# Kernel optimization log

Hardware: AMD Instinct MI355X
Metric: run time of the kernel (lower is better)

The kernel has to match this reference:

```python
import jax, jax.numpy as jnp
import numpy as np

D = 256      # d_model
NH = 8       # heads
HD = D // NH # head dim = 32
NL = 4       # feature levels
NP = 4       # sampling points per head per level
DFF = 1024   # ffn hidden
LAYERS = 6
SHAPES = [(48, 48), (24, 24), (12, 12), (6, 6)]


def setup_inputs() -> dict:
    key = jax.random.key(0)
    ks = jax.random.split(key, 20)
    bs = 2
    inp = {}
    for i, (h, w) in enumerate(SHAPES):
        inp[f"src{i}"] = jax.random.normal(ks[i], (bs, D, h, w), jnp.float32)
        inp[f"pos{i}"] = jax.random.normal(ks[4 + i], (bs, D, h, w), jnp.float32)

    def p(k, shape, s=0.02):
        return jax.random.normal(k, shape, jnp.float32) * s

    inp["level_embed"] = p(ks[8], (NL, D), 1.0)
    inp["Wv"] = p(ks[9], (LAYERS, D, D))
    inp["bv"] = jnp.zeros((LAYERS, D))
    inp["Woff"] = p(ks[10], (LAYERS, D, NH * NL * NP * 2), 0.001)
    inp["boff"] = p(ks[11], (LAYERS, NH * NL * NP * 2), 0.5)
    inp["Wa"] = p(ks[12], (LAYERS, D, NH * NL * NP))
    inp["ba"] = jnp.zeros((LAYERS, NH * NL * NP))
    inp["Wo"] = p(ks[13], (LAYERS, D, D))
    inp["bo"] = jnp.zeros((LAYERS, D))
    inp["g1"] = jnp.ones((LAYERS, D))
    inp["beta1"] = jnp.zeros((LAYERS, D))
    inp["W1"] = p(ks[14], (LAYERS, D, DFF))
    inp["bf1"] = jnp.zeros((LAYERS, DFF))
    inp["W2"] = p(ks[15], (LAYERS, DFF, D))
    inp["bf2"] = jnp.zeros((LAYERS, D))
    inp["g2"] = jnp.ones((LAYERS, D))
    inp["beta2"] = jnp.zeros((LAYERS, D))
    return inp


def _ln(x, g, b):
    m = x.mean(-1, keepdims=True)
    v = ((x - m) ** 2).mean(-1, keepdims=True)
    return (x - m) / jnp.sqrt(v + 1e-5) * g + b


def _bilinear(value, loc, H, W):
    # value: (bs, NH, H*W, HD); loc: (bs, Len, NH, NP, 2) in [0,1]
    # grid_sample, align_corners=False, zero padding
    bs, Len, nh, P, _ = loc.shape
    x = loc[..., 0] * W - 0.5
    y = loc[..., 1] * H - 0.5
    x0 = jnp.floor(x)
    y0 = jnp.floor(y)
    lx = x - x0
    ly = y - y0
    x0i = x0.astype(jnp.int32)
    y0i = y0.astype(jnp.int32)
    out = jnp.zeros((bs, nh, Len, P, value.shape[-1]), value.dtype)
    for dy, dx, w in ((0, 0, (1 - lx) * (1 - ly)), (0, 1, lx * (1 - ly)),
                      (1, 0, (1 - lx) * ly), (1, 1, lx * ly)):
        xi = x0i + dx
        yi = y0i + dy
        valid = (xi >= 0) & (xi < W) & (yi >= 0) & (yi < H)
        idx = jnp.clip(yi, 0, H - 1) * W + jnp.clip(xi, 0, W - 1)  # (bs,Len,NH,P)
        idx_t = idx.transpose(0, 2, 1, 3).reshape(bs, nh, Len * P)
        v = jnp.take_along_axis(value, idx_t[..., None], axis=2)
        v = v.reshape(bs, nh, Len, P, -1)
        wm = (w * valid).transpose(0, 2, 1, 3)  # (bs,NH,Len,P)
        out = out + v * wm[..., None]
    return out


def _msda(q, src, ref, shapes, starts, Wv, bv, Woff, boff, Wa, ba, Wo, bo):
    bs, Len, _ = q.shape
    value = (src @ Wv + bv).reshape(bs, Len, NH, HD)
    off = (q @ Woff + boff).reshape(bs, Len, NH, NL, NP, 2)
    attn = jax.nn.softmax((q @ Wa + ba).reshape(bs, Len, NH, NL * NP), -1)
    attn = attn.reshape(bs, Len, NH, NL, NP)
    acc = jnp.zeros((bs, NH, Len, HD), q.dtype)
    for lv, (H, W) in enumerate(shapes):
        norm = jnp.array([W, H], q.dtype)
        loc = ref[None, :, None, None, :] + off[:, :, :, lv] / norm  # (bs,Len,NH,NP,2)
        v = value[:, starts[lv]:starts[lv] + H * W].transpose(0, 2, 1, 3)
        samp = _bilinear(v, loc, H, W)  # (bs,NH,Len,NP,HD)
        acc = acc + (samp * attn[:, :, :, lv].transpose(0, 2, 1, 3)[..., None]).sum(3)
    return acc.transpose(0, 2, 1, 3).reshape(bs, Len, D) @ Wo + bo


def _encode(srcs, poss, level_embed, Wv, bv, Woff, boff, Wa, ba, Wo, bo,
            g1, beta1, W1, bf1, W2, bf2, g2, beta2):
    shapes = [(s.shape[2], s.shape[3]) for s in srcs]
    bs = srcs[0].shape[0]
    src_flat = jnp.concatenate(
        [s.reshape(bs, D, -1).transpose(0, 2, 1) for s in srcs], 1)
    pos_flat = jnp.concatenate(
        [p.reshape(bs, D, -1).transpose(0, 2, 1) + level_embed[i][None, None]
         for i, p in enumerate(poss)], 1)
    starts = np.cumsum([0] + [h * w for h, w in shapes])[:-1]
    # reference points (masks are all-zero so valid_ratios == 1)
    refs = []
    for (H, W) in shapes:
        ry, rx = jnp.meshgrid(jnp.linspace(0.5, H - 0.5, H) / H,
                              jnp.linspace(0.5, W - 0.5, W) / W, indexing='ij')
        refs.append(jnp.stack([rx.reshape(-1), ry.reshape(-1)], -1))
    ref = jnp.concatenate(refs, 0)  # (Len, 2)

    out = src_flat
    for l in range(LAYERS):
        q = out + pos_flat
        out2 = _msda(q, out, ref, shapes, starts, Wv[l], bv[l], Woff[l],
                     boff[l], Wa[l], ba[l], Wo[l], bo[l])
        out = _ln(out + out2, g1[l], beta1[l])
        h = jax.nn.relu(out @ W1[l] + bf1[l])
        out = _ln(out + h @ W2[l] + bf2[l], g2[l], beta2[l])
    return out, shapes, starts


def reference(src0, src1, src2, src3, pos0, pos1, pos2, pos3, level_embed,
              Wv, bv, Woff, boff, Wa, ba, Wo, bo,
              g1, beta1, W1, bf1, W2, bf2, g2, beta2):
    memory, shapes, starts = _encode(
        [src0, src1, src2, src3], [pos0, pos1, pos2, pos3], level_embed,
        Wv, bv, Woff, boff, Wa, ba, Wo, bo,
        g1, beta1, W1, bf1, W2, bf2, g2, beta2)
    spatial_shapes = jnp.array(shapes, jnp.int32)
    level_start_index = jnp.array(np.asarray(starts), jnp.int32)
    return memory, spatial_shapes, level_start_index
```

## Files before the change

### kernel.cpp

```cpp
#include <hip/hip_runtime.h>
#include <math.h>

#define D_MODEL 256
#define NHEAD 8
#define HDIM 32
#define NLVL 4
#define NPTS 4
#define DFF 1024
#define NLAYERS 6
#define LEN 3060
#define BS 2
#define MROWS (BS * LEN)
#define MPAD 6144

typedef __attribute__((ext_vector_type(8))) short bf16x8;
typedef __attribute__((ext_vector_type(4))) float f32x4;

__device__ __forceinline__ unsigned short f2bf(float f) {
    union { float f; unsigned u; } v; v.f = f;
    unsigned r = v.u + 0x7FFF + ((v.u >> 16) & 1);
    return (unsigned short)(r >> 16);
}
__device__ __forceinline__ float bf2f(unsigned short s) {
    union { unsigned u; float f; } v; v.u = ((unsigned)s) << 16;
    return v.f;
}

#define GLDS(gp, lp) __builtin_amdgcn_global_load_lds(                        \
    (const __attribute__((address_space(1))) void*)(gp),                      \
    (__attribute__((address_space(3))) void*)(lp), 16, 0, 0)

__global__ __launch_bounds__(256) void flatten_kernel(
    const float* __restrict__ s0, const float* __restrict__ s1,
    const float* __restrict__ s2, const float* __restrict__ s3,
    const float* __restrict__ p0, const float* __restrict__ p1,
    const float* __restrict__ p2, const float* __restrict__ p3,
    const float* __restrict__ lemb,
    float* __restrict__ out, unsigned short* __restrict__ outbf,
    unsigned short* __restrict__ qbf, float* __restrict__ pos)
{
    int gid = blockIdx.x * 256 + threadIdx.x;
    if (gid >= MROWS * D_MODEL) return;
    int d  = gid & (D_MODEL - 1);
    int bt = gid >> 8;
    int b  = (bt >= LEN) ? 1 : 0;
    int t  = bt - b * LEN;

    int lv, li, hw;
    const float* sp; const float* pp;
    if (t < 2304)      { lv = 0; li = t;        hw = 2304; sp = s0; pp = p0; }
    else if (t < 2880) { lv = 1; li = t - 2304; hw = 576;  sp = s1; pp = p1; }
    else if (t < 3024) { lv = 2; li = t - 2880; hw = 144;  sp = s2; pp = p2; }
    else               { lv = 3; li = t - 3024; hw = 36;   sp = s3; pp = p3; }

    size_t si = (size_t)(b * D_MODEL + d) * hw + li;
    float v = sp[si];
    float pv = pp[si] + lemb[lv * D_MODEL + d];
    out[gid]   = v;
    outbf[gid] = f2bf(v);
    qbf[gid]   = f2bf(v + pv);
    pos[gid]   = pv;
}

__global__ __launch_bounds__(256) void wconv_kernel(
    const float* __restrict__ Wv, const float* __restrict__ Woff,
    const float* __restrict__ Wa, const float* __restrict__ Wo,
    const float* __restrict__ W1, const float* __restrict__ W2,
    unsigned short* __restrict__ Wv_t, unsigned short* __restrict__ Woffa_t,
    unsigned short* __restrict__ Wo_t, unsigned short* __restrict__ W1_t,
    unsigned short* __restrict__ W2_t)
{
    __shared__ float tile[32][33];
    int bid = blockIdx.x;
    int layer = bid / 736, r = bid % 736;
    const float* src; unsigned short* dst;
    int N, tk, tn, dstRowOff = 0, dstLd;
    if (r < 64)       { src = Wv  + layer*65536;  dst = Wv_t   + layer*65536;  N = 256;  int t2 = r;       tk = t2 >> 3; tn = t2 & 7;  dstLd = 256;  }
    else if (r < 128) { src = Woff+ layer*65536;  dst = Woffa_t+ layer*98304;  N = 256;  int t2 = r - 64;  tk = t2 >> 3; tn = t2 & 7;  dstLd = 256;  }
    else if (r < 160) { src = Wa  + layer*32768;  dst = Woffa_t+ layer*98304;  N = 128;  int t2 = r - 128; tk = t2 >> 2; tn = t2 & 3;  dstLd = 256;  dstRowOff = 256; }
    else if (r < 224) { src = Wo  + layer*65536;  dst = Wo_t   + layer*65536;  N = 256;  int t2 = r - 160; tk = t2 >> 3; tn = t2 & 7;  dstLd = 256;  }
    else if (r < 480) { src = W1  + layer*262144; dst = W1_t   + layer*262144; N = 1024; int t2 = r - 224; tk = t2 >> 5; tn = t2 & 31; dstLd = 256;  }
    else              { src = W2  + layer*262144; dst = W2_t   + layer*262144; N = 256;  int t2 = r - 480; tk = t2 >> 3; tn = t2 & 7;  dstLd = 1024; }
    int k0 = tk * 32, n0 = tn * 32;
    int tx = threadIdx.x & 31, ty = threadIdx.x >> 5;
    #pragma unroll
    for (int i = 0; i < 4; ++i)
        tile[ty + i*8][tx] = src[(size_t)(k0 + ty + i*8) * N + n0 + tx];
    __syncthreads();
    #pragma unroll
    for (int i = 0; i < 4; ++i)
        dst[(size_t)(dstRowOff + n0 + ty + i*8) * dstLd + k0 + tx] =
            f2bf(tile[tx][ty + i*8]);
}

__device__ __forceinline__ void gemm_core(
    const unsigned short* __restrict__ A, const unsigned short* __restrict__ Bt,
    int row0, int col0, int K, char* smem, f32x4 (&acc)[4][2])
{
    const int tid  = threadIdx.x;
    const int lane = tid & 63, wave = tid >> 6;
    const int wm = wave >> 1, wn = wave & 1;
    const int l15 = lane & 15, l4 = lane >> 4;

    const unsigned short* aS[4]; const unsigned short* bS[2];
    int aD[4], bD[2];
    #pragma unroll
    for (int i = 0; i < 4; ++i) {
        int c = i*256 + tid, q = c >> 7, r = c & 127;
        aS[i] = A + (size_t)(row0 + r) * K + q*8;
        aD[i] = c * 16;
    }
    #pragma unroll
    for (int i = 0; i < 2; ++i) {
        int c = i*256 + tid, q = c >> 6, n = c & 63;
        bS[i] = Bt + (size_t)(col0 + n) * K + q*8;
        bD[i] = 16384 + c * 16;
    }

    int aOff[4][2], bOff[2][2];
    #pragma unroll
    for (int mf = 0; mf < 4; ++mf)
        #pragma unroll
        for (int s = 0; s < 2; ++s)
            aOff[mf][s] = ((s*4 + l4)*128 + wm*64 + mf*16 + l15) * 16;
    #pragma unroll
    for (int nf = 0; nf < 2; ++nf)
        #pragma unroll
        for (int s = 0; s < 2; ++s)
            bOff[nf][s] = 16384 + ((s*4 + l4)*64 + wn*32 + nf*16 + l15) * 16;

    #pragma unroll
    for (int i = 0; i < 4; ++i) GLDS(aS[i], smem + aD[i]);
    #pragma unroll
    for (int i = 0; i < 2; ++i) GLDS(bS[i], smem + bD[i]);
    __syncthreads();

    const int nt = K >> 6;
    for (int t = 0; t < nt; ++t) {
        const int bo = (t & 1) * 24576;
        if (t + 1 < nt) {
            const int nbo = ((t + 1) & 1) * 24576;
            const int k0 = (t + 1) << 6;
            #pragma unroll
            for (int i = 0; i < 4; ++i) GLDS(aS[i] + k0, smem + nbo + aD[i]);
            #pragma unroll
            for (int i = 0; i < 2; ++i) GLDS(bS[i] + k0, smem + nbo + bD[i]);
        }
        #pragma unroll
        for (int s = 0; s < 2; ++s) {
            bf16x8 bfr[2];
            #pragma unroll
            for (int nf = 0; nf < 2; ++nf)
                bfr[nf] = *(const bf16x8*)(smem + bo + bOff[nf][s]);
            #pragma unroll
            for (int mf = 0; mf < 4; ++mf) {
                bf16x8 afr = *(const bf16x8*)(smem + bo + aOff[mf][s]);
                #pragma unroll
                for (int nf = 0; nf < 2; ++nf)
                    acc[mf][nf] = __builtin_amdgcn_mfma_f32_16x16x32_bf16(
                        afr, bfr[nf], acc[mf][nf], 0, 0, 0);
            }
        }
        __syncthreads();
    }
}

template<bool RELU, bool OUTBF>
__global__ __launch_bounds__(256) void gemm3(
    const unsigned short* __restrict__ A, const unsigned short* __restrict__ Bt,
    const float* __restrict__ bias, void* __restrict__ Cout, int N, int K)
{
    __shared__ __align__(16) char smem[49152];
    f32x4 acc[4][2] = {};
    const int row0 = blockIdx.y * 128, col0 = blockIdx.x * 64;
    gemm_core(A, Bt, row0, col0, K, smem, acc);

    const int lane = threadIdx.x & 63, wave = threadIdx.x >> 6;
    const int wm = wave >> 1, wn = wave & 1;
    const int l15 = lane & 15, l4 = lane >> 4;
    #pragma unroll
    for (int nf = 0; nf < 2; ++nf) {
        int col = col0 + wn*32 + nf*16 + l15;
        float bb = bias[col];
        #pragma unroll
        for (int mf = 0; mf < 4; ++mf)
            #pragma unroll
            for (int i = 0; i < 4; ++i) {
                int row = row0 + wm*64 + mf*16 + l4*4 + i;
                if (row < MROWS) {
                    float v = acc[mf][nf][i] + bb;
                    if (RELU) v = fmaxf(v, 0.f);
                    if (OUTBF)
                        ((unsigned short*)Cout)[(size_t)row * N + col] = f2bf(v);
                    else
                        ((float*)Cout)[(size_t)row * N + col] = v;
                }
            }
    }
}

__global__ __launch_bounds__(256) void gemm_va(
    const unsigned short* __restrict__ outbf, const unsigned short* __restrict__ qbf,
    const unsigned short* __restrict__ Wv_l, const unsigned short* __restrict__ Woffa_l,
    const float* __restrict__ bv, const float* __restrict__ boff,
    const float* __restrict__ ba,
    unsigned short* __restrict__ valbf, float* __restrict__ offattn)
{
    __shared__ __align__(16) char smem[49152];
    const int bx = blockIdx.x;
    const bool isV = bx < 4;
    const unsigned short* A  = isV ? outbf : qbf;
    const unsigned short* Bt = isV ? Wv_l : Woffa_l;
    const int col0 = isV ? bx * 64 : (bx - 4) * 64;
    const int row0 = blockIdx.y * 128;

    f32x4 acc[4][2] = {};
    gemm_core(A, Bt, row0, col0, 256, smem, acc);

    const int lane = threadIdx.x & 63, wave = threadIdx.x >> 6;
    const int wm = wave >> 1, wn = wave & 1;
    const int l15 = lane & 15, l4 = lane >> 4;
    #pragma unroll
    for (int nf = 0; nf < 2; ++nf) {
        int col = col0 + wn*32 + nf*16 + l15;
        float bb = isV ? bv[col] : (col < 256 ? boff[col] : ba[col - 256]);
        #pragma unroll
        for (int mf = 0; mf < 4; ++mf)
            #pragma unroll
            for (int i = 0; i < 4; ++i) {
                int row = row0 + wm*64 + mf*16 + l4*4 + i;
                if (row < MROWS) {
                    float v = acc[mf][nf][i] + bb;
                    if (isV)
                        valbf[(size_t)row * 256 + col] = f2bf(v);
                    else
                        offattn[(size_t)row * 384 + col] = v;
                }
            }
    }
}

__global__ __launch_bounds__(256) void msda_kernel(
    const unsigned short* __restrict__ value,
    const float* __restrict__ offattn,
    unsigned short* __restrict__ outb)
{
    int gid = blockIdx.x * 256 + threadIdx.x;
    if (gid >= MROWS * NHEAD * 8) return;
    int part = gid & 7;
    int h    = (gid >> 3) & 7;
    int bt   = gid >> 6;
    int b    = (bt >= LEN) ? 1 : 0;
    int t    = bt - b * LEN;

    const float* lg = offattn + (size_t)bt * 384 + 256 + h * 16;
    float w[16];
    float mx = -1e30f;
    #pragma unroll
    for (int j = 0; j < 16; ++j) { w[j] = lg[j]; mx = fmaxf(mx, w[j]); }
    float s = 0.f;
    #pragma unroll
    for (int j = 0; j < 16; ++j) { w[j] = __expf(w[j] - mx); s += w[j]; }
    float inv = 1.f / s;

    int li, Wr;
    if (t < 2304)      { li = t;        Wr = 48; }
    else if (t < 2880) { li = t - 2304; Wr = 24; }
    else if (t < 3024) { li = t - 2880; Wr = 12; }
    else               { li = t - 3024; Wr = 6;  }
    float refx = ((li % Wr) + 0.5f) / (float)Wr;
    float refy = ((li / Wr) + 0.5f) / (float)Wr;

    const float* offp = offattn + (size_t)bt * 384 + h * 32;
    const unsigned short* valbase =
        value + (size_t)b * LEN * D_MODEL + h * HDIM + part * 4;

    const int starts[4] = {0, 2304, 2880, 3024};
    const int Ws[4]     = {48, 24, 12, 6};

    float4 acc = make_float4(0.f, 0.f, 0.f, 0.f);

    #pragma unroll
    for (int lv = 0; lv < NLVL; ++lv) {
        int Wl = Ws[lv];
        int stt = starts[lv];
        float fW = (float)Wl;
        #pragma unroll
        for (int p = 0; p < NPTS; ++p) {
            float ox = offp[(lv * NPTS + p) * 2 + 0];
            float oy = offp[(lv * NPTS + p) * 2 + 1];
            float x = (refx + ox / fW) * fW - 0.5f;
            float y = (refy + oy / fW) * fW - 0.5f;
            float x0f = floorf(x), y0f = floorf(y);
            float lx = x - x0f, ly = y - y0f;
            int x0 = (int)x0f, y0 = (int)y0f;
            float aw = w[lv * NPTS + p] * inv;
            float tw[4] = {(1.f - lx) * (1.f - ly), lx * (1.f - ly),
                           (1.f - lx) * ly,         lx * ly};
            const int dxs[4] = {0, 1, 0, 1};
            const int dys[4] = {0, 0, 1, 1};
            #pragma unroll
            for (int tap = 0; tap < 4; ++tap) {
                int xi = x0 + dxs[tap], yi = y0 + dys[tap];
                bool valid = (xi >= 0) & (xi < Wl) & (yi >= 0) & (yi < Wl);
                int xc = xi < 0 ? 0 : (xi > Wl - 1 ? Wl - 1 : xi);
                int yc = yi < 0 ? 0 : (yi > Wl - 1 ? Wl - 1 : yi);
                int tt = stt + yc * Wl + xc;
                ushort4 vv = *(const ushort4*)(valbase + (size_t)tt * D_MODEL);
                float wt = valid ? aw * tw[tap] : 0.f;
                acc.x += wt * bf2f(vv.x); acc.y += wt * bf2f(vv.y);
                acc.z += wt * bf2f(vv.z); acc.w += wt * bf2f(vv.w);
            }
        }
    }
    ushort4 o = make_ushort4(f2bf(acc.x), f2bf(acc.y), f2bf(acc.z), f2bf(acc.w));
    *(ushort4*)(outb + (size_t)bt * D_MODEL + h * HDIM + part * 4) = o;
}

template<bool WITH_POS>
__global__ __launch_bounds__(256) void add_ln_kernel(
    float* __restrict__ out, unsigned short* __restrict__ outbf,
    const float* __restrict__ add,
    const float* __restrict__ g, const float* __restrict__ be,
    const float* __restrict__ pos, unsigned short* __restrict__ qbf)
{
    int row  = blockIdx.x * 4 + (threadIdx.x >> 6);
    int lane = threadIdx.x & 63;
    if (row >= MROWS) return;

    float4 x = ((const float4*)(out + (size_t)row * D_MODEL))[lane];
    float4 y = ((const float4*)(add + (size_t)row * D_MODEL))[lane];
    x.x += y.x; x.y += y.y; x.z += y.z; x.w += y.w;

    float s  = x.x + x.y + x.z + x.w;
    float ss = x.x * x.x + x.y * x.y + x.z * x.z + x.w * x.w;
    #pragma unroll
    for (int m = 1; m < 64; m <<= 1) {
        s  += __shfl_xor(s, m);
        ss += __shfl_xor(ss, m);
    }
    float mean = s * (1.f / 256.f);
    float var  = ss * (1.f / 256.f) - mean * mean;
    float rstd = rsqrtf(var + 1e-5f);

    float4 gv = ((const float4*)g)[lane];
    float4 bv = ((const float4*)be)[lane];
    float4 o;
    o.x = (x.x - mean) * rstd * gv.x + bv.x;
    o.y = (x.y - mean) * rstd * gv.y + bv.y;
    o.z = (x.z - mean) * rstd * gv.z + bv.z;
    o.w = (x.w - mean) * rstd * gv.w + bv.w;
    ((float4*)(out + (size_t)row * D_MODEL))[lane] = o;
    ((ushort4*)(outbf + (size_t)row * D_MODEL))[lane] =
        make_ushort4(f2bf(o.x), f2bf(o.y), f2bf(o.z), f2bf(o.w));
    if (WITH_POS) {
        float4 pv = ((const float4*)(pos + (size_t)row * D_MODEL))[lane];
        ((ushort4*)(qbf + (size_t)row * D_MODEL))[lane] =
            make_ushort4(f2bf(o.x + pv.x), f2bf(o.y + pv.y),
                         f2bf(o.z + pv.z), f2bf(o.w + pv.w));
    }
}

__global__ void tail_kernel(float* __restrict__ tail)
{
    if (threadIdx.x == 0 && blockIdx.x == 0) {
        const float vals[12] = {48.f, 48.f, 24.f, 24.f, 12.f, 12.f, 6.f, 6.f,
                                0.f, 2304.f, 2880.f, 3024.f};
        #pragma unroll
        for (int i = 0; i < 12; ++i) tail[i] = vals[i];
    }
}

extern "C" void kernel_launch(void* const* d_in, const int* in_sizes, int n_in,
                              void* d_out, int out_size, void* d_ws, size_t ws_size,
                              hipStream_t stream)
{
    const float* SRC[4]; const float* POS[4];
    bool interleaved = (in_sizes[1] == in_sizes[0]);
    if (interleaved) {
        SRC[0] = (const float*)d_in[0]; POS[0] = (const float*)d_in[1];
        SRC[1] = (const float*)d_in[2]; POS[1] = (const float*)d_in[3];
        SRC[2] = (const float*)d_in[4]; POS[2] = (const float*)d_in[5];
        SRC[3] = (const float*)d_in[6]; POS[3] = (const float*)d_in[7];
    } else {
        for (int i = 0; i < 4; ++i) {
            SRC[i] = (const float*)d_in[i];
            POS[i] = (const float*)d_in[4 + i];
        }
    }
    const float* lemb  = (const float*)d_in[8];
    const float* Wv    = (const float*)d_in[9];
    const float* bv    = (const float*)d_in[10];
    const float* Woff  = (const float*)d_in[11];
    const float* boff  = (const float*)d_in[12];
    const float* Wa    = (const float*)d_in[13];
    const float* ba    = (const float*)d_in[14];
    const float* Wo    = (const float*)d_in[15];
    const float* bo    = (const float*)d_in[16];
    const float* g1    = (const float*)d_in[17];
    const float* beta1 = (const float*)d_in[18];
    const float* W1    = (const float*)d_in[19];
    const float* bf1   = (const float*)d_in[20];
    const float* W2    = (const float*)d_in[21];
    const float* bf2   = (const float*)d_in[22];
    const float* g2    = (const float*)d_in[23];
    const float* beta2 = (const float*)d_in[24];

    float* out = (float*)d_out;

    char* ws = (char*)d_ws;
    float* pos     = (float*)ws;                   ws += (size_t)MPAD * 256 * 4;
    float* offattn = (float*)ws;                   ws += (size_t)MPAD * 384 * 4;
    float* tmp     = (float*)ws;                   ws += (size_t)MPAD * 256 * 4;
    unsigned short* qbf    = (unsigned short*)ws;  ws += (size_t)MPAD * 256 * 2;
    unsigned short* outbf  = (unsigned short*)ws;  ws += (size_t)MPAD * 256 * 2;
    unsigned short* msdabf = (unsigned short*)ws;  ws += (size_t)MPAD * 256 * 2;
    unsigned short* valbf  = (unsigned short*)ws;  ws += (size_t)MPAD * 256 * 2;
    unsigned short* hbuf   = (unsigned short*)ws;  ws += (size_t)MPAD * 1024 * 2;
    unsigned short* Wv_t    = (unsigned short*)ws; ws += (size_t)6 * 65536 * 2;
    unsigned short* Woffa_t = (unsigned short*)ws; ws += (size_t)6 * 98304 * 2;
    unsigned short* Wo_t    = (unsigned short*)ws; ws += (size_t)6 * 65536 * 2;
    unsigned short* W1_t    = (unsigned short*)ws; ws += (size_t)6 * 262144 * 2;
    unsigned short* W2_t    = (unsigned short*)ws; ws += (size_t)6 * 262144 * 2;

    wconv_kernel<<<6 * 736, 256, 0, stream>>>(Wv, Woff, Wa, Wo, W1, W2,
                                              Wv_t, Woffa_t, Wo_t, W1_t, W2_t);

    const int nElem = MROWS * D_MODEL;
    flatten_kernel<<<(nElem + 255) / 256, 256, 0, stream>>>(
        SRC[0], SRC[1], SRC[2], SRC[3], POS[0], POS[1], POS[2], POS[3],
        lemb, out, outbf, qbf, pos);

    const dim3 gVA(10, MPAD / 128);
    const dim3 g256(4, MPAD / 128);
    const dim3 g1024(16, MPAD / 128);
    const int gLN = MROWS / 4;

    for (int l = 0; l < NLAYERS; ++l) {
        const unsigned short* Wv_l    = Wv_t    + (size_t)l * 65536;
        const unsigned short* Woffa_l = Woffa_t + (size_t)l * 98304;
        const unsigned short* Wo_l    = Wo_t    + (size_t)l * 65536;
        const unsigned short* W1_l    = W1_t    + (size_t)l * 262144;
        const unsigned short* W2_l    = W2_t    + (size_t)l * 262144;

        gemm_va<<<gVA, 256, 0, stream>>>(
            outbf, qbf, Wv_l, Woffa_l, bv + l * 256, boff + l * 256,
            ba + l * 128, valbf, offattn);

        msda_kernel<<<(MROWS * NHEAD * 8 + 255) / 256, 256, 0, stream>>>(
            valbf, offattn, msdabf);

        gemm3<false, false><<<g256, 256, 0, stream>>>(
            msdabf, Wo_l, bo + l * 256, tmp, 256, 256);

        add_ln_kernel<false><<<gLN, 256, 0, stream>>>(
            out, outbf, tmp, g1 + l * 256, beta1 + l * 256, pos, qbf);

        gemm3<true, true><<<g1024, 256, 0, stream>>>(
            outbf, W1_l, bf1 + l * DFF, hbuf, 1024, 256);

        gemm3<false, false><<<g256, 256, 0, stream>>>(
            hbuf, W2_l, bf2 + l * 256, tmp, 256, 1024);

        add_ln_kernel<true><<<gLN, 256, 0, stream>>>(
            out, outbf, tmp, g2 + l * 256, beta2 + l * 256, pos, qbf);
    }

    tail_kernel<<<1, 64, 0, stream>>>(out + (size_t)MROWS * D_MODEL);
}
```

Before: 731.8 us.

## Use 64x64 full-K GEMM tiles, split-K FFN2, swizzled grids, softmax in epilogue

Replaces the double-buffered 128x64 GEMM core with 64x64 tiles that load a whole K=256 slab into LDS at once. The tile count doubles so more blocks fill the CUs. Block indices are swizzled across the grid, and FFN2 is split along K into two partial outputs that the LayerNorm kernel sums. The attention softmax moves from the sampling kernel into the value/offset GEMM epilogue using 16-lane shuffles. In exchange it uses more LDS per block, gives up load/compute overlap within a block, and adds an extra partial buffer read.

```diff
diff --git a/kernel.cpp b/kernel.cpp
--- a/kernel.cpp
+++ b/kernel.cpp
@@ -12,6 +12,7 @@
 #define BS 2
 #define MROWS (BS * LEN)
 #define MPAD 6144
+#define PSTRIDE ((size_t)MPAD * 256)
 
 typedef __attribute__((ext_vector_type(8))) short bf16x8;
 typedef __attribute__((ext_vector_type(4))) float f32x4;
@@ -29,6 +30,14 @@
 #define GLDS(gp, lp) __builtin_amdgcn_global_load_lds(                        \
     (const __attribute__((address_space(1))) void*)(gp),                      \
     (__attribute__((address_space(3))) void*)(lp), 16, 0, 0)
+
+__device__ __forceinline__ void swz_xy(int& tx, int& ty) {
+    const int gx = gridDim.x;
+    const int id = blockIdx.y * gx + blockIdx.x;
+    const int q  = (gx * gridDim.y) >> 3;
+    const int L  = (id & 7) * q + (id >> 3);
+    ty = L / gx; tx = L - ty * gx;
+}
 
 __global__ __launch_bounds__(256) void flatten_kernel(
     const float* __restrict__ s0, const float* __restrict__ s1,
@@ -93,87 +102,60 @@
             f2bf(tile[tx][ty + i*8]);
 }
 
-__device__ __forceinline__ void gemm_core(
-    const unsigned short* __restrict__ A, const unsigned short* __restrict__ Bt,
-    int row0, int col0, int K, char* smem, f32x4 (&acc)[4][2])
-{
-    const int tid  = threadIdx.x;
-    const int lane = tid & 63, wave = tid >> 6;
+template<int NSTAGE>
+__device__ __forceinline__ void gemm_fk_core(
+    const unsigned short* __restrict__ A, int lda,
+    const unsigned short* __restrict__ Bt, int ldb,
+    int row0, int col0, char* smem, f32x4 (&acc)[2][2])
+{
+    const int tid = threadIdx.x, lane = tid & 63, wave = tid >> 6;
     const int wm = wave >> 1, wn = wave & 1;
     const int l15 = lane & 15, l4 = lane >> 4;
 
-    const unsigned short* aS[4]; const unsigned short* bS[2];
-    int aD[4], bD[2];
-    #pragma unroll
-    for (int i = 0; i < 4; ++i) {
-        int c = i*256 + tid, q = c >> 7, r = c & 127;
-        aS[i] = A + (size_t)(row0 + r) * K + q*8;
-        aD[i] = c * 16;
-    }
-    #pragma unroll
-    for (int i = 0; i < 2; ++i) {
-        int c = i*256 + tid, q = c >> 6, n = c & 63;
-        bS[i] = Bt + (size_t)(col0 + n) * K + q*8;
-        bD[i] = 16384 + c * 16;
-    }
-
-    int aOff[4][2], bOff[2][2];
-    #pragma unroll
-    for (int mf = 0; mf < 4; ++mf)
-        #pragma unroll
-        for (int s = 0; s < 2; ++s)
-            aOff[mf][s] = ((s*4 + l4)*128 + wm*64 + mf*16 + l15) * 16;
-    #pragma unroll
-    for (int nf = 0; nf < 2; ++nf)
-        #pragma unroll
-        for (int s = 0; s < 2; ++s)
-            bOff[nf][s] = 16384 + ((s*4 + l4)*64 + wn*32 + nf*16 + l15) * 16;
-
-    #pragma unroll
-    for (int i = 0; i < 4; ++i) GLDS(aS[i], smem + aD[i]);
-    #pragma unroll
-    for (int i = 0; i < 2; ++i) GLDS(bS[i], smem + bD[i]);
-    __syncthreads();
-
-    const int nt = K >> 6;
-    for (int t = 0; t < nt; ++t) {
-        const int bo = (t & 1) * 24576;
-        if (t + 1 < nt) {
-            const int nbo = ((t + 1) & 1) * 24576;
-            const int k0 = (t + 1) << 6;
+    #pragma unroll 1
+    for (int st = 0; st < NSTAGE; ++st) {
+        if (st) __syncthreads();
+        const int kb = st * 256;
+        #pragma unroll
+        for (int i = 0; i < 8; ++i) {
+            int c = i * 256 + tid, q = c >> 6, r = c & 63;
+            GLDS(A + (size_t)(row0 + r) * lda + kb + q * 8, smem + c * 16);
+        }
+        #pragma unroll
+        for (int i = 0; i < 8; ++i) {
+            int c = i * 256 + tid, q = c >> 6, n = c & 63;
+            GLDS(Bt + (size_t)(col0 + n) * ldb + kb + q * 8, smem + 32768 + c * 16);
+        }
+        __syncthreads();
+        #pragma unroll
+        for (int kf = 0; kf < 8; ++kf) {
+            const int q = kf * 4 + l4;
+            bf16x8 av[2], bv[2];
+            av[0] = *(const bf16x8*)(smem + (q*64 + wm*32      + l15) * 16);
+            av[1] = *(const bf16x8*)(smem + (q*64 + wm*32 + 16 + l15) * 16);
+            bv[0] = *(const bf16x8*)(smem + 32768 + (q*64 + wn*32      + l15) * 16);
+            bv[1] = *(const bf16x8*)(smem + 32768 + (q*64 + wn*32 + 16 + l15) * 16);
             #pragma unroll
-            for (int i = 0; i < 4; ++i) GLDS(aS[i] + k0, smem + nbo + aD[i]);
-            #pragma unroll
-            for (int i = 0; i < 2; ++i) GLDS(bS[i] + k0, smem + nbo + bD[i]);
-        }
-        #pragma unroll
-        for (int s = 0; s < 2; ++s) {
-            bf16x8 bfr[2];
-            #pragma unroll
-            for (int nf = 0; nf < 2; ++nf)
-                bfr[nf] = *(const bf16x8*)(smem + bo + bOff[nf][s]);
-            #pragma unroll
-            for (int mf = 0; mf < 4; ++mf) {
-                bf16x8 afr = *(const bf16x8*)(smem + bo + aOff[mf][s]);
+            for (int mf = 0; mf < 2; ++mf)
                 #pragma unroll
                 for (int nf = 0; nf < 2; ++nf)
                     acc[mf][nf] = __builtin_amdgcn_mfma_f32_16x16x32_bf16(
-                        afr, bfr[nf], acc[mf][nf], 0, 0, 0);
-            }
+                        av[mf], bv[nf], acc[mf][nf], 0, 0, 0);
         }
-        __syncthreads();
     }
 }
 
 template<bool RELU, bool OUTBF>
-__global__ __launch_bounds__(256) void gemm3(
+__global__ __launch_bounds__(256) void gemm_std(
     const unsigned short* __restrict__ A, const unsigned short* __restrict__ Bt,
-    const float* __restrict__ bias, void* __restrict__ Cout, int N, int K)
-{
-    __shared__ __align__(16) char smem[49152];
-    f32x4 acc[4][2] = {};
-    const int row0 = blockIdx.y * 128, col0 = blockIdx.x * 64;
-    gemm_core(A, Bt, row0, col0, K, smem, acc);
+    const float* __restrict__ bias, void* __restrict__ Cout, int N)
+{
+    __shared__ __align__(16) char smem[65536];
+    int tx, ty; swz_xy(tx, ty);
+    const int row0 = ty * 64, col0 = tx * 64;
+
+    f32x4 acc[2][2] = {};
+    gemm_fk_core<1>(A, 256, Bt, 256, row0, col0, smem, acc);
 
     const int lane = threadIdx.x & 63, wave = threadIdx.x >> 6;
     const int wm = wave >> 1, wn = wave & 1;
@@ -183,10 +165,10 @@
         int col = col0 + wn*32 + nf*16 + l15;
         float bb = bias[col];
         #pragma unroll
-        for (int mf = 0; mf < 4; ++mf)
+        for (int mf = 0; mf < 2; ++mf)
             #pragma unroll
             for (int i = 0; i < 4; ++i) {
-                int row = row0 + wm*64 + mf*16 + l4*4 + i;
+                int row = row0 + wm*32 + mf*16 + l4*4 + i;
                 if (row < MROWS) {
                     float v = acc[mf][nf][i] + bb;
                     if (RELU) v = fmaxf(v, 0.f);
@@ -206,36 +188,82 @@
     const float* __restrict__ ba,
     unsigned short* __restrict__ valbf, float* __restrict__ offattn)
 {
-    __shared__ __align__(16) char smem[49152];
-    const int bx = blockIdx.x;
-    const bool isV = bx < 4;
+    __shared__ __align__(16) char smem[65536];
+    int tx, ty; swz_xy(tx, ty);
+    const bool isV = tx < 4;
     const unsigned short* A  = isV ? outbf : qbf;
     const unsigned short* Bt = isV ? Wv_l : Woffa_l;
-    const int col0 = isV ? bx * 64 : (bx - 4) * 64;
-    const int row0 = blockIdx.y * 128;
-
-    f32x4 acc[4][2] = {};
-    gemm_core(A, Bt, row0, col0, 256, smem, acc);
+    const int col0 = isV ? tx * 64 : (tx - 4) * 64;
+    const int row0 = ty * 64;
+
+    f32x4 acc[2][2] = {};
+    gemm_fk_core<1>(A, 256, Bt, 256, row0, col0, smem, acc);
 
     const int lane = threadIdx.x & 63, wave = threadIdx.x >> 6;
     const int wm = wave >> 1, wn = wave & 1;
     const int l15 = lane & 15, l4 = lane >> 4;
     #pragma unroll
     for (int nf = 0; nf < 2; ++nf) {
-        int col = col0 + wn*32 + nf*16 + l15;
+        int base = col0 + wn*32 + nf*16;
+        int col  = base + l15;
         float bb = isV ? bv[col] : (col < 256 ? boff[col] : ba[col - 256]);
-        #pragma unroll
-        for (int mf = 0; mf < 4; ++mf)
+        const bool isAttn = (!isV) && (base >= 256);
+        #pragma unroll
+        for (int mf = 0; mf < 2; ++mf)
             #pragma unroll
             for (int i = 0; i < 4; ++i) {
-                int row = row0 + wm*64 + mf*16 + l4*4 + i;
+                int row = row0 + wm*32 + mf*16 + l4*4 + i;
+                float v = acc[mf][nf][i] + bb;
+                if (isAttn) {
+                    float mx = v;
+                    #pragma unroll
+                    for (int m = 1; m < 16; m <<= 1)
+                        mx = fmaxf(mx, __shfl_xor(mx, m));
+                    float e = __expf(v - mx);
+                    float s = e;
+                    #pragma unroll
+                    for (int m = 1; m < 16; m <<= 1)
+                        s += __shfl_xor(s, m);
+                    v = e / s;
+                }
                 if (row < MROWS) {
-                    float v = acc[mf][nf][i] + bb;
                     if (isV)
                         valbf[(size_t)row * 256 + col] = f2bf(v);
                     else
                         offattn[(size_t)row * 384 + col] = v;
                 }
+            }
+    }
+}
+
+__global__ __launch_bounds__(256) void gemm_ffn2(
+    const unsigned short* __restrict__ hbuf, const unsigned short* __restrict__ W2_t,
+    const float* __restrict__ bias, float* __restrict__ part)
+{
+    __shared__ __align__(16) char smem[65536];
+    int tx, ty; swz_xy(tx, ty);
+    const int ct = tx & 3, s = tx >> 2;
+    const int row0 = ty * 64, col0 = ct * 64;
+
+    f32x4 acc[2][2] = {};
+    gemm_fk_core<2>(hbuf + s * 512, 1024, W2_t + s * 512, 1024,
+                    row0, col0, smem, acc);
+
+    float* dst = part + (size_t)s * PSTRIDE;
+    const int lane = threadIdx.x & 63, wave = threadIdx.x >> 6;
+    const int wm = wave >> 1, wn = wave & 1;
+    const int l15 = lane & 15, l4 = lane >> 4;
+    #pragma unroll
+    for (int nf = 0; nf < 2; ++nf) {
+        int col = col0 + wn*32 + nf*16 + l15;
+        float bb = (s == 0) ? bias[col] : 0.f;
+        #pragma unroll
+        for (int mf = 0; mf < 2; ++mf)
+            #pragma unroll
+            for (int i = 0; i < 4; ++i) {
+                int row = row0 + wm*32 + mf*16 + l4*4 + i;
+                if (row < MROWS)
+                    dst[(size_t)row * 256 + col] = acc[mf][nf][i] + bb;
             }
     }
 }
@@ -253,16 +281,6 @@
     int b    = (bt >= LEN) ? 1 : 0;
     int t    = bt - b * LEN;
 
-    const float* lg = offattn + (size_t)bt * 384 + 256 + h * 16;
-    float w[16];
-    float mx = -1e30f;
-    #pragma unroll
-    for (int j = 0; j < 16; ++j) { w[j] = lg[j]; mx = fmaxf(mx, w[j]); }
-    float s = 0.f;
-    #pragma unroll
-    for (int j = 0; j < 16; ++j) { w[j] = __expf(w[j] - mx); s += w[j]; }
-    float inv = 1.f / s;
-
     int li, Wr;
     if (t < 2304)      { li = t;        Wr = 48; }
     else if (t < 2880) { li = t - 2304; Wr = 24; }
@@ -271,12 +289,13 @@
     float refx = ((li % Wr) + 0.5f) / (float)Wr;
     float refy = ((li / Wr) + 0.5f) / (float)Wr;
 
+    const int starts[4] = {0, 2304, 2880, 3024};
+    const int Ws[4]     = {48, 24, 12, 6};
+
+    const float* lg   = offattn + (size_t)bt * 384 + 256 + h * 16;
     const float* offp = offattn + (size_t)bt * 384 + h * 32;
     const unsigned short* valbase =
         value + (size_t)b * LEN * D_MODEL + h * HDIM + part * 4;
-
-    const int starts[4] = {0, 2304, 2880, 3024};
-    const int Ws[4]     = {48, 24, 12, 6};
 
     float4 acc = make_float4(0.f, 0.f, 0.f, 0.f);
 
@@ -289,12 +308,12 @@
         for (int p = 0; p < NPTS; ++p) {
             float ox = offp[(lv * NPTS + p) * 2 + 0];
             float oy = offp[(lv * NPTS + p) * 2 + 1];
+            float aw = lg[lv * NPTS + p];
             float x = (refx + ox / fW) * fW - 0.5f;
             float y = (refy + oy / fW) * fW - 0.5f;
             float x0f = floorf(x), y0f = floorf(y);
             float lx = x - x0f, ly = y - y0f;
             int x0 = (int)x0f, y0 = (int)y0f;
-            float aw = w[lv * NPTS + p] * inv;
             float tw[4] = {(1.f - lx) * (1.f - ly), lx * (1.f - ly),
                            (1.f - lx) * ly,         lx * ly};
             const int dxs[4] = {0, 1, 0, 1};
@@ -317,10 +336,10 @@
     *(ushort4*)(outb + (size_t)bt * D_MODEL + h * HDIM + part * 4) = o;
 }
 
-template<bool WITH_POS>
+template<int NPART, bool WITH_POS>
 __global__ __launch_bounds__(256) void add_ln_kernel(
     float* __restrict__ out, unsigned short* __restrict__ outbf,
-    const float* __restrict__ add,
+    const float* __restrict__ part,
     const float* __restrict__ g, const float* __restrict__ be,
     const float* __restrict__ pos, unsigned short* __restrict__ qbf)
 {
@@ -329,8 +348,12 @@
     if (row >= MROWS) return;
 
     float4 x = ((const float4*)(out + (size_t)row * D_MODEL))[lane];
-    float4 y = ((const float4*)(add + (size_t)row * D_MODEL))[lane];
+    float4 y = ((const float4*)(part + (size_t)row * D_MODEL))[lane];
     x.x += y.x; x.y += y.y; x.z += y.z; x.w += y.w;
+    if (NPART == 2) {
+        float4 z = ((const float4*)(part + PSTRIDE + (size_t)row * D_MODEL))[lane];
+        x.x += z.x; x.y += z.y; x.z += z.z; x.w += z.w;
+    }
 
     float s  = x.x + x.y + x.z + x.w;
     float ss = x.x * x.x + x.y * x.y + x.z * x.z + x.w * x.w;
@@ -411,7 +434,7 @@
     char* ws = (char*)d_ws;
     float* pos     = (float*)ws;                   ws += (size_t)MPAD * 256 * 4;
     float* offattn = (float*)ws;                   ws += (size_t)MPAD * 384 * 4;
-    float* tmp     = (float*)ws;                   ws += (size_t)MPAD * 256 * 4;
+    float* part    = (float*)ws;                   ws += 2 * PSTRIDE * 4;
     unsigned short* qbf    = (unsigned short*)ws;  ws += (size_t)MPAD * 256 * 2;
     unsigned short* outbf  = (unsigned short*)ws;  ws += (size_t)MPAD * 256 * 2;
     unsigned short* msdabf = (unsigned short*)ws;  ws += (size_t)MPAD * 256 * 2;
@@ -431,9 +454,11 @@
         SRC[0], SRC[1], SRC[2], SRC[3], POS[0], POS[1], POS[2], POS[3],
         lemb, out, outbf, qbf, pos);
 
-    const dim3 gVA(10, MPAD / 128);
-    const dim3 g256(4, MPAD / 128);
-    const dim3 g1024(16, MPAD / 128);
+    const int GY = MPAD / 64;
+    const dim3 gVA(10, GY);
+    const dim3 gWo(4, GY);
+    const dim3 gF1(16, GY);
+    const dim3 gF2(8, GY);
     const int gLN = MROWS / 4;
 
     for (int l = 0; l < NLAYERS; ++l) {
@@ -450,20 +475,19 @@
         msda_kernel<<<(MROWS * NHEAD * 8 + 255) / 256, 256, 0, stream>>>(
             valbf, offattn, msdabf);
 
-        gemm3<false, false><<<g256, 256, 0, stream>>>(
-            msdabf, Wo_l, bo + l * 256, tmp, 256, 256);
-
-        add_ln_kernel<false><<<gLN, 256, 0, stream>>>(
-            out, outbf, tmp, g1 + l * 256, beta1 + l * 256, pos, qbf);
-
-        gemm3<true, true><<<g1024, 256, 0, stream>>>(
-            outbf, W1_l, bf1 + l * DFF, hbuf, 1024, 256);
-
-        gemm3<false, false><<<g256, 256, 0, stream>>>(
-            hbuf, W2_l, bf2 + l * 256, tmp, 256, 1024);
-
-        add_ln_kernel<true><<<gLN, 256, 0, stream>>>(
-            out, outbf, tmp, g2 + l * 256, beta2 + l * 256, pos, qbf);
+        gemm_std<false, false><<<gWo, 256, 0, stream>>>(
+            msdabf, Wo_l, bo + l * 256, part, 256);
+
+        add_ln_kernel<1, false><<<gLN, 256, 0, stream>>>(
+            out, outbf, part, g1 + l * 256, beta1 + l * 256, pos, qbf);
+
+        gemm_std<true, true><<<gF1, 256, 0, stream>>>(
+            outbf, W1_l, bf1 + l * DFF, hbuf, 1024);
+
+        gemm_ffn2<<<gF2, 256, 0, stream>>>(hbuf, W2_l, bf2 + l * 256, part);
+
+        add_ln_kernel<2, true><<<gLN, 256, 0, stream>>>(
+            out, outbf, part, g2 + l * 256, beta2 + l * 256, pos, qbf);
     }
 
     tail_kernel<<<1, 64, 0, stream>>>(out + (size_t)MROWS * D_MODEL);
```

After: 754.3 us. 3.1% more time.
